# Kernel optimization log

Measured on AMD Instinct MI355X. Metric: run time of the kernel, lower is better.

The kernel has to match this reference:

```python
import jax, jax.numpy as jnp
import numpy as np

N_NODES = 4096
N_EDGES = 524288
IN_DIM = 6
EMB_N = 4
EMB_D = 8
EDGE_D = 1
HID = 64
N_HEADS = 4
LN_EPS = 1e-5


def _layernorm(h, g, b):
    m = jnp.mean(h, axis=-1, keepdims=True)
    v = jnp.mean(jnp.square(h - m), axis=-1, keepdims=True)
    return (h - m) * jax.lax.rsqrt(v + LN_EPS) * g + b


def setup_inputs() -> dict:
    key = jax.random.key(0)
    ks = jax.random.split(key, 16)
    s = lambda fan_in: 1.0 / np.sqrt(fan_in)
    inp = {
        'x': jax.random.normal(ks[0], (N_NODES, IN_DIM), jnp.float32),
        'edge_attr': jax.random.uniform(ks[1], (N_EDGES, EDGE_D), jnp.float32),
        'entity_emb': jax.random.normal(ks[2], (EMB_N, EMB_D), jnp.float32),
        'lin1_w': jax.random.uniform(ks[3], (HID, IN_DIM + EMB_D + EDGE_D), jnp.float32, -s(15), s(15)),
        'lin1_b': jnp.zeros((HID,), jnp.float32),
        'lay_w': jax.random.uniform(ks[4], (HID, HID), jnp.float32, -s(HID), s(HID)),
        'lay_b': jnp.zeros((HID,), jnp.float32),
        'ln_g': jnp.ones((HID,), jnp.float32),
        'ln_b': jnp.zeros((HID,), jnp.float32),
        'in_proj_w': jax.random.uniform(ks[5], (3 * HID, HID), jnp.float32, -s(HID), s(HID)),
        'in_proj_b': jnp.zeros((3 * HID,), jnp.float32),
        'out_proj_w': jax.random.uniform(ks[6], (HID, HID), jnp.float32, -s(HID), s(HID)),
        'out_proj_b': jnp.zeros((HID,), jnp.float32),
        'an_g': jnp.ones((HID,), jnp.float32),
        'an_b': jnp.zeros((HID,), jnp.float32),
        'out_w': jax.random.uniform(ks[7], (HID, HID), jnp.float32, -s(HID), s(HID)),
        'out_b': jnp.zeros((HID,), jnp.float32),
        'edge_index': jax.random.randint(ks[8], (2, N_EDGES), 0, N_NODES, jnp.int64),
        'entity_type': jax.random.randint(ks[9], (N_NODES,), 0, EMB_N, jnp.int64),
    }
    return inp


def reference(x, edge_attr, entity_emb, lin1_w, lin1_b, lay_w, lay_b, ln_g, ln_b,
              in_proj_w, in_proj_b, out_proj_w, out_proj_b, an_g, an_b, out_w, out_b,
              edge_index, entity_type):
    # --- EmbedConv ---
    # concat node features with entity embedding: [N, 6+8]
    xe = jnp.concatenate([x, entity_emb[entity_type]], axis=-1)
    src, dst = edge_index[0], edge_index[1]
    # gather source nodes + edge attr: [E, 15]
    msg = jnp.concatenate([xe[src], edge_attr], axis=-1)
    msg = _layernorm(jax.nn.relu(msg @ lin1_w.T + lin1_b), ln_g, ln_b)
    # layer_N = 1 extra layer, shared LayerNorm
    msg = _layernorm(jax.nn.relu(msg @ lay_w.T + lay_b), ln_g, ln_b)
    # scatter-add aggregate into destination nodes: [N, 64]
    h = jax.ops.segment_sum(msg, dst, num_segments=N_NODES)
    # --- MultiheadAttention over all nodes as one sequence (eval: no dropout) ---
    qkv = h @ in_proj_w.T + in_proj_b  # [N, 3H]
    q, k, v = jnp.split(qkv, 3, axis=-1)
    hd = HID // N_HEADS
    q = q.reshape(N_NODES, N_HEADS, hd).transpose(1, 0, 2)  # [h, n, d]
    k = k.reshape(N_NODES, N_HEADS, hd).transpose(1, 0, 2)
    v = v.reshape(N_NODES, N_HEADS, hd).transpose(1, 0, 2)
    scores = jnp.einsum('hnd,hmd->hnm', q, k) / np.sqrt(hd)
    attn = jax.nn.softmax(scores, axis=-1)
    o = jnp.einsum('hnm,hmd->hnd', attn, v).transpose(1, 0, 2).reshape(N_NODES, HID)
    o = o @ out_proj_w.T + out_proj_b
    h = _layernorm(h + o, an_g, an_b)
    # --- output layer ---
    return h @ out_w.T + out_b
```

## Files before the change

kernel.cpp:

```cpp
#include <hip/hip_runtime.h>

#define N_NODES 4096
#define N_EDGES 524288
#define HID 64

typedef short short8 __attribute__((ext_vector_type(8)));
typedef float f32x4 __attribute__((ext_vector_type(4)));
typedef float f32x16 __attribute__((ext_vector_type(16)));

__device__ __forceinline__ float bcastf(float v, int l) {
    return __int_as_float(__builtin_amdgcn_readlane(__float_as_int(v), l));
}

__device__ __forceinline__ void wave_sum2(float& a, float& b) {
    #pragma unroll
    for (int off = 32; off > 0; off >>= 1) {
        a += __shfl_xor(a, off, 64);
        b += __shfl_xor(b, off, 64);
    }
}

__device__ __forceinline__ short f2bf(float f) {
    unsigned u = __float_as_uint(f);
    u = u + 0x7FFFu + ((u >> 16) & 1u);
    return (short)(u >> 16);
}
__device__ __forceinline__ float bf2f(short s) {
    return __uint_as_float(((unsigned)(unsigned short)s) << 16);
}
__device__ __forceinline__ void split_cheap(float f, short& hi, short& lo) {
    unsigned u = __float_as_uint(f);
    unsigned hb = u & 0xffff0000u;
    float lof = f - __uint_as_float(hb);
    hi = (short)(u >> 16);
    lo = (short)(__float_as_uint(lof) >> 16);
}

__global__ void hist_prep(const float* __restrict__ x, const float* __restrict__ emb,
                          const int* __restrict__ etype, const int* __restrict__ ei,
                          const float* __restrict__ w1, const float* __restrict__ b1,
                          const float* __restrict__ w2, const float* __restrict__ lng,
                          const float* __restrict__ lnb, const float* __restrict__ b2,
                          const float* __restrict__ ipw,
                          float* __restrict__ A1, int* __restrict__ cnt, int* __restrict__ rank,
                          unsigned short* __restrict__ w2fh, unsigned short* __restrict__ w2fl,
                          unsigned short* __restrict__ ipfh, unsigned short* __restrict__ ipfl,
                          float* __restrict__ b2p, float* __restrict__ w14p) {
    int tid = blockIdx.x * 256 + threadIdx.x;
    int d = ei[N_EDGES + tid];
    rank[tid] = atomicAdd(&cnt[d], 1);
    if (tid < N_NODES * 64) {
        int n = tid >> 6, f = tid & 63;
        const float* wr = w1 + f * 15;
        float acc = b1[f];
        #pragma unroll
        for (int k = 0; k < 6; k++) acc = fmaf(x[n * 6 + k], wr[k], acc);
        int e = etype[n];
        #pragma unroll
        for (int k = 0; k < 8; k++) acc = fmaf(emb[e * 8 + k], wr[6 + k], acc);
        A1[tid] = acc;
    }
    if (tid < 4096) {
        int idx = tid >> 9, ln = (tid >> 3) & 63, j = tid & 7;
        int mm = ln & 15, qq = ln >> 4;
        int g = idx >> 1, tt = idx & 1;
        int col = tt * 32 + qq * 8 + j;
        float w = w2[(g * 16 + mm) * 64 + col] * lng[col];
        short hi = f2bf(w);
        w2fh[tid] = (unsigned short)hi;
        w2fl[tid] = (unsigned short)f2bf(w - bf2f(hi));
    }
    if (tid < 12288) {
        int idx = tid >> 9, ln = (tid >> 3) & 63, j = tid & 7;
        int mm = ln & 15, qq = ln >> 4;
        int og = idx >> 1, tt = idx & 1;
        float w = ipw[(og * 16 + mm) * 64 + tt * 32 + qq * 8 + j];
        short hi = f2bf(w);
        ipfh[tid] = (unsigned short)hi;
        ipfl[tid] = (unsigned short)f2bf(w - bf2f(hi));
    }
    if (tid < 64) {
        float acc = b2[tid];
        for (int c = 0; c < 64; c++) acc = fmaf(w2[tid * 64 + c], lnb[c], acc);
        b2p[tid] = acc;
        w14p[tid] = w1[tid * 15 + 14];
    }
}

__global__ void __launch_bounds__(256) scatter_scan(
        const int* __restrict__ cnt, const int* __restrict__ ei,
        const float* __restrict__ edge_attr, const int* __restrict__ rank,
        int* __restrict__ bnd,
        int* __restrict__ ssrc, float* __restrict__ sea) {
    __shared__ int lbnd[4096];
    __shared__ int wsum[4];
    int t = threadIdx.x;
    int base = t * 16;
    int v16[16];
    int T = 0;
    #pragma unroll
    for (int j = 0; j < 16; j++) { v16[j] = cnt[base + j]; T += v16[j]; }
    int inc = T;
    int l = t & 63;
    #pragma unroll
    for (int off = 1; off < 64; off <<= 1) {
        int v = __shfl_up(inc, off, 64);
        if (l >= off) inc += v;
    }
    if (l == 63) wsum[t >> 6] = inc;
    __syncthreads();
    int wo = 0;
    for (int w = 0; w < (t >> 6); w++) wo += wsum[w];
    int run = wo + inc - T;
    #pragma unroll
    for (int j = 0; j < 16; j++) {
        lbnd[base + j] = run;
        run += v16[j];
    }
    if (blockIdx.x == 0) {
        #pragma unroll
        for (int j = 0; j < 16; j++) bnd[base + j] = lbnd[base + j];
        if (t == 255) bnd[4096] = run;
    }
    __syncthreads();
    int e = blockIdx.x * 256 + t;
    int d = ei[N_EDGES + e];
    int pos = lbnd[d] + rank[e];
    ssrc[pos] = ei[e];
    sea[pos] = edge_attr[e];
}

__global__ void __launch_bounds__(256, 4) edge_gather_mfma(
        const float* __restrict__ A1,
        const int* __restrict__ ssrc, const float* __restrict__ sea,
        const int* __restrict__ bnd,
        const unsigned short* __restrict__ w2fh, const unsigned short* __restrict__ w2fl,
        const float* __restrict__ w14p, const float* __restrict__ b2p,
        const float* __restrict__ lg, const float* __restrict__ lb,
        float* __restrict__ h) {
    __shared__ uint4 lw2h4[512];
    __shared__ uint4 lw2l4[512];
    int tid = threadIdx.x;
    {
        const uint4* gh = (const uint4*)w2fh;
        const uint4* gl = (const uint4*)w2fl;
        lw2h4[tid] = gh[tid];
        lw2h4[tid + 256] = gh[tid + 256];
        lw2l4[tid] = gl[tid];
        lw2l4[tid + 256] = gl[tid + 256];
    }
    const unsigned short* lw2h = (const unsigned short*)lw2h4;
    const unsigned short* lw2l = (const unsigned short*)lw2l4;

    int lane = tid & 63;
    int wv = tid >> 6;
    int m = lane & 15;
    int q = lane >> 4;

    float w14f[16];
    {
        float4 wa = *(const float4*)(w14p + q * 8);
        float4 wb = *(const float4*)(w14p + q * 8 + 4);
        float4 wc = *(const float4*)(w14p + 32 + q * 8);
        float4 wd = *(const float4*)(w14p + 32 + q * 8 + 4);
        w14f[0] = wa.x; w14f[1] = wa.y; w14f[2] = wa.z; w14f[3] = wa.w;
        w14f[4] = wb.x; w14f[5] = wb.y; w14f[6] = wb.z; w14f[7] = wb.w;
        w14f[8] = wc.x; w14f[9] = wc.y; w14f[10] = wc.z; w14f[11] = wc.w;
        w14f[12] = wd.x; w14f[13] = wd.y; w14f[14] = wd.z; w14f[15] = wd.w;
    }
    float b2v[4];
    #pragma unroll
    for (int g = 0; g < 4; g++) b2v[g] = b2p[g * 16 + m];
    float lgv = lg[lane], lbv = lb[lane];

    int node = blockIdx.x * 4 + wv;
    int start = bnd[node], end = bnd[node + 1];
    int ntiles = (end - start + 15) >> 4;
    float acc[4] = {0.f, 0.f, 0.f, 0.f};
    __syncthreads();

    int srcn = 0; float eav = 0.f;
    if (ntiles > 0) {
        int ec = start + m; if (ec >= end) ec = end - 1;
        srcn = ssrc[ec]; eav = sea[ec];
    }
    for (int t = 0; t < ntiles; t++) {
        int base = start + t * 16;
        const float* ar = A1 + srcn * 64 + q * 8;
        float4 va = *(const float4*)(ar);
        float4 vb = *(const float4*)(ar + 4);
        float4 vc = *(const float4*)(ar + 32);
        float4 vd = *(const float4*)(ar + 36);
        int srcn_n = srcn; float eav_n = eav;
        if (t + 1 < ntiles) {
            int e2 = base + 16 + m; if (e2 >= end) e2 = end - 1;
            srcn_n = ssrc[e2]; eav_n = sea[e2];
        }
        float v[16] = {va.x, va.y, va.z, va.w, vb.x, vb.y, vb.z, vb.w,
                       vc.x, vc.y, vc.z, vc.w, vd.x, vd.y, vd.z, vd.w};
        float s = 0.f, s2 = 0.f;
        #pragma unroll
        for (int j = 0; j < 16; j++) {
            float u = fmaxf(fmaf(w14f[j], eav, v[j]), 0.f);
            v[j] = u;
            s += u;
            s2 = fmaf(u, u, s2);
        }
        s += __shfl_xor(s, 16, 64);  s2 += __shfl_xor(s2, 16, 64);
        s += __shfl_xor(s, 32, 64);  s2 += __shfl_xor(s2, 32, 64);
        float mean = s * (1.f / 64.f);
        float var = s2 * (1.f / 64.f) - mean * mean;
        float rs = rsqrtf(var + 1e-5f);
        float a0 = -mean * rs;
        short8 a2h[2], a2l[2];
        #pragma unroll
        for (int t2 = 0; t2 < 2; t2++)
            #pragma unroll
            for (int j = 0; j < 8; j++) {
                short hi, lo;
                split_cheap(fmaf(v[t2 * 8 + j], rs, a0), hi, lo);
                a2h[t2][j] = hi;
                a2l[t2][j] = lo;
            }
        int ob = (t >> 20);
        float s_[4] = {0, 0, 0, 0}, s2_[4] = {0, 0, 0, 0};
        float t2v[4][4];
        #pragma unroll
        for (int g = 0; g < 4; g++) {
            f32x4 c = {0.f, 0.f, 0.f, 0.f};
            #pragma unroll
            for (int t2 = 0; t2 < 2; t2++) {
                short8 bh = *(const short8*)(lw2h + ((g * 2 + t2) * 64 + lane + ob) * 8);
                short8 bl = *(const short8*)(lw2l + ((g * 2 + t2) * 64 + lane + ob) * 8);
                c = __builtin_amdgcn_mfma_f32_16x16x32_bf16(a2l[t2], bh, c, 0, 0, 0);
                c = __builtin_amdgcn_mfma_f32_16x16x32_bf16(a2h[t2], bl, c, 0, 0, 0);
                c = __builtin_amdgcn_mfma_f32_16x16x32_bf16(a2h[t2], bh, c, 0, 0, 0);
            }
            #pragma unroll
            for (int i = 0; i < 4; i++) {
                float vv = fmaxf(c[i] + b2v[g], 0.f);
                t2v[g][i] = vv;
                s_[i] += vv;
                s2_[i] = fmaf(vv, vv, s2_[i]);
            }
        }
        #pragma unroll
        for (int off = 1; off < 16; off <<= 1)
            #pragma unroll
            for (int i = 0; i < 4; i++) {
                s_[i] += __shfl_xor(s_[i], off, 64);
                s2_[i] += __shfl_xor(s2_[i], off, 64);
            }
        #pragma unroll
        for (int i = 0; i < 4; i++) {
            float mean2 = s_[i] * (1.f / 64.f);
            float var2 = s2_[i] * (1.f / 64.f) - mean2 * mean2;
            float rs2 = rsqrtf(var2 + 1e-5f);
            bool valid = (base + q * 4 + i) < end;
            #pragma unroll
            for (int g = 0; g < 4; g++) {
                float z = (t2v[g][i] - mean2) * rs2;
                if (valid) acc[g] += z;
            }
        }
        srcn = srcn_n; eav = eav_n;
    }
    #pragma unroll
    for (int g = 0; g < 4; g++) {
        acc[g] += __shfl_xor(acc[g], 16, 64);
        acc[g] += __shfl_xor(acc[g], 32, 64);
    }
    float a01 = (q & 1) ? acc[1] : acc[0];
    float a23 = (q & 1) ? acc[3] : acc[2];
    float av = (q & 2) ? a23 : a01;
    h[node * 64 + lane] = lgv * av + (float)(end - start) * lbv;
}

__global__ void __launch_bounds__(256) qkv_mfma(
        const float* __restrict__ h, const float* __restrict__ b,
        const unsigned short* __restrict__ ipfh, const unsigned short* __restrict__ ipfl,
        unsigned short* __restrict__ qhp, unsigned short* __restrict__ qlp,
        unsigned short* __restrict__ khp, unsigned short* __restrict__ klp,
        unsigned short* __restrict__ vT) {
    int lane = threadIdx.x & 63;
    int wv = threadIdx.x >> 6;
    int m = lane & 15;
    int q = lane >> 4;
    int wid = blockIdx.x * 4 + wv;
    int tile = wid / 12;
    int og = wid - tile * 12;
    short8 bh[2], bl[2];
    #pragma unroll
    for (int t = 0; t < 2; t++) {
        bh[t] = *(const short8*)(ipfh + ((og * 2 + t) * 64 + lane) * 8);
        bl[t] = *(const short8*)(ipfl + ((og * 2 + t) * 64 + lane) * 8);
    }
    f32x4 c = {0.f, 0.f, 0.f, 0.f};
    #pragma unroll
    for (int t = 0; t < 2; t++) {
        const float* hr = h + (tile * 16 + m) * 64 + t * 32 + q * 8;
        float4 f0 = *(const float4*)hr;
        float4 f1 = *(const float4*)(hr + 4);
        float av8[8] = {f0.x, f0.y, f0.z, f0.w, f1.x, f1.y, f1.z, f1.w};
        short8 ah, al;
        #pragma unroll
        for (int j = 0; j < 8; j++) {
            short hi, lo;
            split_cheap(av8[j], hi, lo);
            ah[j] = hi;
            al[j] = lo;
        }
        c = __builtin_amdgcn_mfma_f32_16x16x32_bf16(al, bh[t], c, 0, 0, 0);
        c = __builtin_amdgcn_mfma_f32_16x16x32_bf16(ah, bl[t], c, 0, 0, 0);
        c = __builtin_amdgcn_mfma_f32_16x16x32_bf16(ah, bh[t], c, 0, 0, 0);
    }
    int o = og * 16 + m;
    float bias = b[o];
    #pragma unroll
    for (int r = 0; r < 4; r++) {
        int node = tile * 16 + q * 4 + r;
        float val = c[r] + bias;
        if (og < 4) {
            float aq = val * (0.25f * 1.44269504f);
            size_t idx = ((size_t)(og * N_NODES + node)) * 16 + m;
            short hi = f2bf(aq);
            qhp[idx] = (unsigned short)hi;
            qlp[idx] = (unsigned short)f2bf(aq - bf2f(hi));
        } else if (og < 8) {
            size_t idx = ((size_t)((og - 4) * N_NODES + node)) * 16 + m;
            short hi = f2bf(val);
            khp[idx] = (unsigned short)hi;
            klp[idx] = (unsigned short)f2bf(val - bf2f(hi));
        } else {
            int feat = (og - 8) * 16 + m;
            vT[(size_t)feat * N_NODES + node] = (unsigned short)f2bf(val);
        }
    }
}

__global__ void __launch_bounds__(256) attn_mfma(
        const unsigned short* __restrict__ qhp, const unsigned short* __restrict__ qlp,
        const unsigned short* __restrict__ khp, const unsigned short* __restrict__ klp,
        const unsigned short* __restrict__ vT,
        float* __restrict__ part_o, float* __restrict__ part_ml) {
    int lane = threadIdx.x & 63;
    int wv = threadIdx.x >> 6;
    int l31 = lane & 31;
    int hi = lane >> 5;
    const short8 vones = {0x3F80, 0x3F80, 0x3F80, 0x3F80, 0x3F80, 0x3F80, 0x3F80, 0x3F80};

    int wid = blockIdx.x * 4 + wv;
    int kc = wid & 7;
    int wqt = (wid >> 3) & 127;
    int head = wid >> 10;

    int qrow = wqt * 32 + l31;
    short8 aqh = *(const short8*)(qhp + ((size_t)(head * N_NODES + qrow)) * 16 + hi * 8);
    short8 aql = *(const short8*)(qlp + ((size_t)(head * N_NODES + qrow)) * 16 + hi * 8);

    const unsigned short* khb = khp + (size_t)head * N_NODES * 16;
    const unsigned short* klb = klp + (size_t)head * N_NODES * 16;
    const unsigned short* vtb = vT + (size_t)(head * 16 + (l31 & 15)) * N_NODES;

    float mS = -3e38f;
    f32x16 Ot = {0.f, 0.f, 0.f, 0.f, 0.f, 0.f, 0.f, 0.f,
                 0.f, 0.f, 0.f, 0.f, 0.f, 0.f, 0.f, 0.f};

    size_t koff = ((size_t)(kc * 512 + l31)) * 16 + hi * 8;
    short8 bkh = *(const short8*)(khb + koff);
    short8 bkl = *(const short8*)(klb + koff);

    for (int bb = 0; bb < 16; bb++) {
        int n0 = kc * 512 + bb * 32;
        int nbb = (bb + 1 < 16) ? (bb + 1) : 15;
        size_t koffn = ((size_t)(kc * 512 + nbb * 32 + l31)) * 16 + hi * 8;
        short8 nkh = *(const short8*)(khb + koffn);
        short8 nkl = *(const short8*)(klb + koffn);
        f32x16 S = {0.f, 0.f, 0.f, 0.f, 0.f, 0.f, 0.f, 0.f,
                    0.f, 0.f, 0.f, 0.f, 0.f, 0.f, 0.f, 0.f};
        S = __builtin_amdgcn_mfma_f32_32x32x16_bf16(bkh, aql, S, 0, 0, 0);
        S = __builtin_amdgcn_mfma_f32_32x32x16_bf16(bkl, aqh, S, 0, 0, 0);
        S = __builtin_amdgcn_mfma_f32_32x32x16_bf16(bkh, aqh, S, 0, 0, 0);
        float mr = S[0];
        #pragma unroll
        for (int r = 1; r < 16; r++) mr = fmaxf(mr, S[r]);
        mr = fmaxf(mr, __shfl_xor(mr, 32, 64));
        if (!__all(mr <= mS)) {
            float mn = fmaxf(mS, mr);
            float alpha = exp2f(mS - mn);
            mS = mn;
            #pragma unroll
            for (int r = 0; r < 9; r++) Ot[r] *= alpha;
        }
        float p[16];
        #pragma unroll
        for (int r = 0; r < 16; r++) p[r] = exp2f(S[r] - mS);
        unsigned w0, w1, w2, w3, u0, u1, u2, u3;
        asm("v_cvt_pk_bf16_f32 %0, %1, %2" : "=v"(w0) : "v"(p[0]), "v"(p[1]));
        asm("v_cvt_pk_bf16_f32 %0, %1, %2" : "=v"(w1) : "v"(p[2]), "v"(p[3]));
        asm("v_cvt_pk_bf16_f32 %0, %1, %2" : "=v"(w2) : "v"(p[4]), "v"(p[5]));
        asm("v_cvt_pk_bf16_f32 %0, %1, %2" : "=v"(w3) : "v"(p[6]), "v"(p[7]));
        asm("v_cvt_pk_bf16_f32 %0, %1, %2" : "=v"(u0) : "v"(p[8]), "v"(p[9]));
        asm("v_cvt_pk_bf16_f32 %0, %1, %2" : "=v"(u1) : "v"(p[10]), "v"(p[11]));
        asm("v_cvt_pk_bf16_f32 %0, %1, %2" : "=v"(u2) : "v"(p[12]), "v"(p[13]));
        asm("v_cvt_pk_bf16_f32 %0, %1, %2" : "=v"(u3) : "v"(p[14]), "v"(p[15]));
        asm("v_permlane32_swap_b32 %0, %1" : "+v"(w0), "+v"(w2));
        asm("v_permlane32_swap_b32 %0, %1" : "+v"(w1), "+v"(w3));
        asm("v_permlane32_swap_b32 %0, %1" : "+v"(u0), "+v"(u2));
        asm("v_permlane32_swap_b32 %0, %1" : "+v"(u1), "+v"(u3));
        union { unsigned u[4]; short8 s; } pf0, pf1;
        pf0.u[0] = w0; pf0.u[1] = w1; pf0.u[2] = w2; pf0.u[3] = w3;
        pf1.u[0] = u0; pf1.u[1] = u1; pf1.u[2] = u2; pf1.u[3] = u3;
        short8 v0, v1;
        if (l31 < 16) {
            v0 = *(const short8*)(vtb + n0 + hi * 8);
            v1 = *(const short8*)(vtb + n0 + 16 + hi * 8);
        } else if (l31 == 16) {
            v0 = vones; v1 = vones;
        } else {
            v0 = (short8)0; v1 = (short8)0;
        }
        Ot = __builtin_amdgcn_mfma_f32_32x32x16_bf16(v0, pf0.s, Ot, 0, 0, 0);
        Ot = __builtin_amdgcn_mfma_f32_32x32x16_bf16(v1, pf1.s, Ot, 0, 0, 0);
        bkh = nkh; bkl = nkl;
    }
    int qt16 = wqt * 2 + (l31 >> 4);
    int qi = l31 & 15;
    size_t pb = ((size_t)(head * 8 + kc) * 256 + qt16) * 256;
    f32x4 o0 = {Ot[0], Ot[1], Ot[2], Ot[3]};
    f32x4 o1 = {Ot[4], Ot[5], Ot[6], Ot[7]};
    *(f32x4*)(part_o + pb + qi * 16 + hi * 4) = o0;
    *(f32x4*)(part_o + pb + qi * 16 + 8 + hi * 4) = o1;
    if (lane < 32) {
        size_t mb = ((size_t)(head * 8 + kc) * 256 + qt16) * 32;
        part_ml[mb + qi] = mS;
        part_ml[mb + 16 + qi] = Ot[8];
    }
}

__global__ void post_kernel(const float* __restrict__ h,
                            const float* __restrict__ part_o, const float* __restrict__ part_ml,
                            const float* __restrict__ opw, const float* __restrict__ opb,
                            const float* __restrict__ ag, const float* __restrict__ ab,
                            const float* __restrict__ ow, const float* __restrict__ ob,
                            float* __restrict__ out) {
    __shared__ float wl1[64 * 65];
    __shared__ float wl2[64 * 65];
    for (int i = threadIdx.x; i < 4096; i += blockDim.x) {
        int r = i >> 6, c = i & 63;
        wl1[r * 65 + c] = opw[i];
        wl2[r * 65 + c] = ow[i];
    }
    __syncthreads();
    int lane = threadIdx.x & 63;
    int n = blockIdx.x * 4 + (threadIdx.x >> 6);
    int j = lane;
    int head = j >> 4, d = j & 15;
    int qt = n >> 4, qi = n & 15;
    float M = -3e38f, L = 0.f, Ov = 0.f;
    #pragma unroll
    for (int c = 0; c < 8; c++) {
        size_t base = ((size_t)(head * 8 + c) * 256 + qt);
        float mc = part_ml[base * 32 + qi];
        float lc = part_ml[base * 32 + 16 + qi];
        float ov = part_o[base * 256 + qi * 16 + d];
        if (mc > M) {
            float sc = exp2f(M - mc);
            M = mc;
            L = L * sc + lc;
            Ov = Ov * sc + ov;
        } else {
            float sc = exp2f(mc - M);
            L = fmaf(lc, sc, L);
            Ov = fmaf(ov, sc, Ov);
        }
    }
    float oj = Ov / L;
    float acc = opb[j];
    #pragma unroll
    for (int k = 0; k < 64; k++) acc = fmaf(wl1[j * 65 + k], bcastf(oj, k), acc);
    float r = h[n * 64 + j] + acc;
    float s = r, s2 = r * r;
    wave_sum2(s, s2);
    float mean = s * (1.f / 64.f);
    float var = s2 * (1.f / 64.f) - mean * mean;
    float hn = (r - mean) * rsqrtf(var + 1e-5f) * ag[j] + ab[j];
    float acc2 = ob[j];
    #pragma unroll
    for (int k = 0; k < 64; k++) acc2 = fmaf(wl2[j * 65 + k], bcastf(hn, k), acc2);
    out[n * 64 + j] = acc2;
}

extern "C" void kernel_launch(void* const* d_in, const int* in_sizes, int n_in,
                              void* d_out, int out_size, void* d_ws, size_t ws_size,
                              hipStream_t stream) {
    const float* x        = (const float*)d_in[0];
    const float* edge_attr= (const float*)d_in[1];
    const float* emb      = (const float*)d_in[2];
    const float* lin1_w   = (const float*)d_in[3];
    const float* lin1_b   = (const float*)d_in[4];
    const float* lay_w    = (const float*)d_in[5];
    const float* lay_b    = (const float*)d_in[6];
    const float* ln_g     = (const float*)d_in[7];
    const float* ln_b     = (const float*)d_in[8];
    const float* ipw      = (const float*)d_in[9];
    const float* ipb      = (const float*)d_in[10];
    const float* opw      = (const float*)d_in[11];
    const float* opb      = (const float*)d_in[12];
    const float* ang      = (const float*)d_in[13];
    const float* anb      = (const float*)d_in[14];
    const float* ow       = (const float*)d_in[15];
    const float* ob       = (const float*)d_in[16];
    const int*   ei       = (const int*)d_in[17];
    const int*   et       = (const int*)d_in[18];

    char* wsb = (char*)d_ws;
    size_t off = 0;
    float* A1             = (float*)(wsb + off);          off += 1048576;
    float* h              = (float*)(wsb + off);          off += 1048576;
    unsigned short* qhp   = (unsigned short*)(wsb + off); off += 524288;
    unsigned short* qlp   = (unsigned short*)(wsb + off); off += 524288;
    unsigned short* khp   = (unsigned short*)(wsb + off); off += 524288;
    unsigned short* klp   = (unsigned short*)(wsb + off); off += 524288;
    unsigned short* vT    = (unsigned short*)(wsb + off); off += 524288;
    float* part_o         = (float*)(wsb + off);          off += 8388608;
    float* part_ml        = (float*)(wsb + off);          off += 1048576;
    int*   cnt            = (int*)(wsb + off);            off += 16384;
    int*   bnd            = (int*)(wsb + off);            off += 16388;
    off = (off + 255) & ~(size_t)255;
    int*   rank           = (int*)(wsb + off);            off += 2097152;
    int*   ssrc           = (int*)(wsb + off);            off += 2097152;
    float* sea            = (float*)(wsb + off);          off += 2097152;
    unsigned short* w2fh  = (unsigned short*)(wsb + off); off += 8192;
    unsigned short* w2fl  = (unsigned short*)(wsb + off); off += 8192;
    unsigned short* ipfh  = (unsigned short*)(wsb + off); off += 24576;
    unsigned short* ipfl  = (unsigned short*)(wsb + off); off += 24576;
    float* b2p            = (float*)(wsb + off);          off += 256;
    float* w14p           = (float*)(wsb + off);          off += 256;

    (void)hipMemsetAsync(cnt, 0, 4096 * sizeof(int), stream);
    hist_prep<<<2048, 256, 0, stream>>>(x, emb, et, ei, lin1_w, lin1_b, lay_w, ln_g, ln_b,
                                        lay_b, ipw, A1, cnt, rank, w2fh, w2fl, ipfh, ipfl,
                                        b2p, w14p);
    scatter_scan<<<2048, 256, 0, stream>>>(cnt, ei, edge_attr, rank, bnd, ssrc, sea);
    edge_gather_mfma<<<1024, 256, 0, stream>>>(A1, ssrc, sea, bnd, w2fh, w2fl,
                                               w14p, b2p, ln_g, ln_b, h);
    qkv_mfma<<<768, 256, 0, stream>>>(h, ipb, ipfh, ipfl, qhp, qlp, khp, klp, vT);
    attn_mfma<<<1024, 256, 0, stream>>>(qhp, qlp, khp, klp, vT, part_o, part_ml);
    post_kernel<<<1024, 256, 0, stream>>>(h, part_o, part_ml, opw, opb, ang, anb, ow, ob,
                                          (float*)d_out);
}
```

Baseline: 224.7 us.

## Restructure edge gather MFMA to transposed layout with persistent node loop

The edge kernel now swaps the MFMA operand order so each output column holds one edge, which lets the second LayerNorm reduce across lanes once per tile instead of four times, and accumulates 16 features per lane. The A1 row gather for the next tile is prefetched one iteration ahead. bf16 hi/lo splitting uses packed v_cvt_pk_bf16_f32, and the scan reads counts with int4 loads. The grid shrinks to 768 blocks looping over nodes, with launch bounds lowered to 3 blocks per SM. The larger accumulator arrays and the prefetch raise register pressure, and writing h only from m==0 lanes produces narrow scalar stores.

```diff
diff --git a/kernel.cpp b/kernel.cpp
--- a/kernel.cpp
+++ b/kernel.cpp
@@ -34,6 +34,23 @@
     float lof = f - __uint_as_float(hb);
     hi = (short)(u >> 16);
     lo = (short)(__float_as_uint(lof) >> 16);
+}
+
+__device__ __forceinline__ void pack_plane8(const float* vv, short8& ah, short8& al) {
+    union { unsigned u[4]; short8 s; } Uh, Ul;
+    #pragma unroll
+    for (int i = 0; i < 4; i++) {
+        unsigned hw;
+        asm("v_cvt_pk_bf16_f32 %0, %1, %2" : "=v"(hw) : "v"(vv[2 * i]), "v"(vv[2 * i + 1]));
+        float he = __uint_as_float(hw << 16);
+        float ho = __uint_as_float(hw & 0xffff0000u);
+        float le = vv[2 * i] - he;
+        float lo_ = vv[2 * i + 1] - ho;
+        unsigned lw;
+        asm("v_cvt_pk_bf16_f32 %0, %1, %2" : "=v"(lw) : "v"(le), "v"(lo_));
+        Uh.u[i] = hw; Ul.u[i] = lw;
+    }
+    ah = Uh.s; al = Ul.s;
 }
 
 __global__ void hist_prep(const float* __restrict__ x, const float* __restrict__ emb,
@@ -99,7 +116,12 @@
     int v16[16];
     int T = 0;
     #pragma unroll
-    for (int j = 0; j < 16; j++) { v16[j] = cnt[base + j]; T += v16[j]; }
+    for (int j4 = 0; j4 < 4; j4++) {
+        int4 c4 = ((const int4*)cnt)[t * 4 + j4];
+        v16[j4 * 4 + 0] = c4.x; v16[j4 * 4 + 1] = c4.y;
+        v16[j4 * 4 + 2] = c4.z; v16[j4 * 4 + 3] = c4.w;
+        T += c4.x + c4.y + c4.z + c4.w;
+    }
     int inc = T;
     int l = t & 63;
     #pragma unroll
@@ -130,7 +152,7 @@
     sea[pos] = edge_attr[e];
 }
 
-__global__ void __launch_bounds__(256, 4) edge_gather_mfma(
+__global__ void __launch_bounds__(256, 3) edge_gather_mfma(
         const float* __restrict__ A1,
         const int* __restrict__ ssrc, const float* __restrict__ sea,
         const int* __restrict__ bnd,
@@ -168,112 +190,117 @@
         w14f[8] = wc.x; w14f[9] = wc.y; w14f[10] = wc.z; w14f[11] = wc.w;
         w14f[12] = wd.x; w14f[13] = wd.y; w14f[14] = wd.z; w14f[15] = wd.w;
     }
-    float b2v[4];
-    #pragma unroll
-    for (int g = 0; g < 4; g++) b2v[g] = b2p[g * 16 + m];
-    float lgv = lg[lane], lbv = lb[lane];
-
-    int node = blockIdx.x * 4 + wv;
-    int start = bnd[node], end = bnd[node + 1];
-    int ntiles = (end - start + 15) >> 4;
-    float acc[4] = {0.f, 0.f, 0.f, 0.f};
+    float b2v[16];
+    #pragma unroll
+    for (int g = 0; g < 4; g++) {
+        float4 bb = *(const float4*)(b2p + g * 16 + q * 4);
+        b2v[g * 4 + 0] = bb.x; b2v[g * 4 + 1] = bb.y;
+        b2v[g * 4 + 2] = bb.z; b2v[g * 4 + 3] = bb.w;
+    }
     __syncthreads();
 
-    int srcn = 0; float eav = 0.f;
-    if (ntiles > 0) {
-        int ec = start + m; if (ec >= end) ec = end - 1;
-        srcn = ssrc[ec]; eav = sea[ec];
-    }
-    for (int t = 0; t < ntiles; t++) {
-        int base = start + t * 16;
-        const float* ar = A1 + srcn * 64 + q * 8;
-        float4 va = *(const float4*)(ar);
-        float4 vb = *(const float4*)(ar + 4);
-        float4 vc = *(const float4*)(ar + 32);
-        float4 vd = *(const float4*)(ar + 36);
-        int srcn_n = srcn; float eav_n = eav;
-        if (t + 1 < ntiles) {
-            int e2 = base + 16 + m; if (e2 >= end) e2 = end - 1;
-            srcn_n = ssrc[e2]; eav_n = sea[e2];
-        }
-        float v[16] = {va.x, va.y, va.z, va.w, vb.x, vb.y, vb.z, vb.w,
-                       vc.x, vc.y, vc.z, vc.w, vd.x, vd.y, vd.z, vd.w};
-        float s = 0.f, s2 = 0.f;
-        #pragma unroll
-        for (int j = 0; j < 16; j++) {
-            float u = fmaxf(fmaf(w14f[j], eav, v[j]), 0.f);
-            v[j] = u;
-            s += u;
-            s2 = fmaf(u, u, s2);
-        }
-        s += __shfl_xor(s, 16, 64);  s2 += __shfl_xor(s2, 16, 64);
-        s += __shfl_xor(s, 32, 64);  s2 += __shfl_xor(s2, 32, 64);
-        float mean = s * (1.f / 64.f);
-        float var = s2 * (1.f / 64.f) - mean * mean;
-        float rs = rsqrtf(var + 1e-5f);
-        float a0 = -mean * rs;
-        short8 a2h[2], a2l[2];
-        #pragma unroll
-        for (int t2 = 0; t2 < 2; t2++)
+    for (int node = blockIdx.x * 4 + wv; node < N_NODES; node += 3072) {
+        int start = bnd[node], end = bnd[node + 1];
+        int ntiles = (end - start + 15) >> 4;
+        float acc[16];
+        #pragma unroll
+        for (int i = 0; i < 16; i++) acc[i] = 0.f;
+
+        int srcn = 0; float eav = 0.f;
+        float4 va = {0,0,0,0}, vb = {0,0,0,0}, vc = {0,0,0,0}, vd = {0,0,0,0};
+        if (ntiles > 0) {
+            int ec = start + m; if (ec >= end) ec = end - 1;
+            srcn = ssrc[ec]; eav = sea[ec];
+            const float* ar = A1 + srcn * 64 + q * 8;
+            va = *(const float4*)(ar);
+            vb = *(const float4*)(ar + 4);
+            vc = *(const float4*)(ar + 32);
+            vd = *(const float4*)(ar + 36);
+        }
+        for (int t = 0; t < ntiles; t++) {
+            int base = start + t * 16;
+            float v[16] = {va.x, va.y, va.z, va.w, vb.x, vb.y, vb.z, vb.w,
+                           vc.x, vc.y, vc.z, vc.w, vd.x, vd.y, vd.z, vd.w};
+            float eavc = eav;
+            if (t + 1 < ntiles) {
+                int e2 = base + 16 + m; if (e2 >= end) e2 = end - 1;
+                int srcn2 = ssrc[e2]; eav = sea[e2];
+                const float* ar2 = A1 + srcn2 * 64 + q * 8;
+                va = *(const float4*)(ar2);
+                vb = *(const float4*)(ar2 + 4);
+                vc = *(const float4*)(ar2 + 32);
+                vd = *(const float4*)(ar2 + 36);
+            }
+            float s = 0.f, s2 = 0.f;
             #pragma unroll
-            for (int j = 0; j < 8; j++) {
-                short hi, lo;
-                split_cheap(fmaf(v[t2 * 8 + j], rs, a0), hi, lo);
-                a2h[t2][j] = hi;
-                a2l[t2][j] = lo;
+            for (int j = 0; j < 16; j++) {
+                float u = fmaxf(fmaf(w14f[j], eavc, v[j]), 0.f);
+                v[j] = u;
+                s += u;
+                s2 = fmaf(u, u, s2);
             }
-        int ob = (t >> 20);
-        float s_[4] = {0, 0, 0, 0}, s2_[4] = {0, 0, 0, 0};
-        float t2v[4][4];
-        #pragma unroll
-        for (int g = 0; g < 4; g++) {
-            f32x4 c = {0.f, 0.f, 0.f, 0.f};
+            s += __shfl_xor(s, 16, 64);  s2 += __shfl_xor(s2, 16, 64);
+            s += __shfl_xor(s, 32, 64);  s2 += __shfl_xor(s2, 32, 64);
+            float mean = s * (1.f / 64.f);
+            float var = s2 * (1.f / 64.f) - mean * mean;
+            float rs = rsqrtf(var + 1e-5f);
+            float a0 = -mean * rs;
             #pragma unroll
-            for (int t2 = 0; t2 < 2; t2++) {
-                short8 bh = *(const short8*)(lw2h + ((g * 2 + t2) * 64 + lane + ob) * 8);
-                short8 bl = *(const short8*)(lw2l + ((g * 2 + t2) * 64 + lane + ob) * 8);
-                c = __builtin_amdgcn_mfma_f32_16x16x32_bf16(a2l[t2], bh, c, 0, 0, 0);
-                c = __builtin_amdgcn_mfma_f32_16x16x32_bf16(a2h[t2], bl, c, 0, 0, 0);
-                c = __builtin_amdgcn_mfma_f32_16x16x32_bf16(a2h[t2], bh, c, 0, 0, 0);
+            for (int j = 0; j < 16; j++) v[j] = fmaf(v[j], rs, a0);
+            short8 a2h[2], a2l[2];
+            pack_plane8(v, a2h[0], a2l[0]);
+            pack_plane8(v + 8, a2h[1], a2l[1]);
+            int ob = (t >> 20);
+            float s_ = 0.f, s2_ = 0.f;
+            float t2v[16];
+            #pragma unroll
+            for (int g = 0; g < 4; g++) {
+                f32x4 c = {0.f, 0.f, 0.f, 0.f};
+                #pragma unroll
+                for (int t2 = 0; t2 < 2; t2++) {
+                    short8 bh = *(const short8*)(lw2h + ((g * 2 + t2) * 64 + lane + ob) * 8);
+                    short8 bl = *(const short8*)(lw2l + ((g * 2 + t2) * 64 + lane + ob) * 8);
+                    c = __builtin_amdgcn_mfma_f32_16x16x32_bf16(bh, a2l[t2], c, 0, 0, 0);
+                    c = __builtin_amdgcn_mfma_f32_16x16x32_bf16(bl, a2h[t2], c, 0, 0, 0);
+                    c = __builtin_amdgcn_mfma_f32_16x16x32_bf16(bh, a2h[t2], c, 0, 0, 0);
+                }
+                #pragma unroll
+                for (int r = 0; r < 4; r++) {
+                    float vv = fmaxf(c[r] + b2v[g * 4 + r], 0.f);
+                    t2v[g * 4 + r] = vv;
+                    s_ += vv;
+                    s2_ = fmaf(vv, vv, s2_);
+                }
             }
-            #pragma unroll
-            for (int i = 0; i < 4; i++) {
-                float vv = fmaxf(c[i] + b2v[g], 0.f);
-                t2v[g][i] = vv;
-                s_[i] += vv;
-                s2_[i] = fmaf(vv, vv, s2_[i]);
+            s_ += __shfl_xor(s_, 16, 64);  s2_ += __shfl_xor(s2_, 16, 64);
+            s_ += __shfl_xor(s_, 32, 64);  s2_ += __shfl_xor(s2_, 32, 64);
+            float mean2 = s_ * (1.f / 64.f);
+            float var2 = s2_ * (1.f / 64.f) - mean2 * mean2;
+            float rs2 = rsqrtf(var2 + 1e-5f);
+            float a02 = -mean2 * rs2;
+            if (base + m < end) {
+                #pragma unroll
+                for (int i = 0; i < 16; i++) acc[i] += fmaf(t2v[i], rs2, a02);
             }
         }
         #pragma unroll
         for (int off = 1; off < 16; off <<= 1)
             #pragma unroll
-            for (int i = 0; i < 4; i++) {
-                s_[i] += __shfl_xor(s_[i], off, 64);
-                s2_[i] += __shfl_xor(s2_[i], off, 64);
-            }
-        #pragma unroll
-        for (int i = 0; i < 4; i++) {
-            float mean2 = s_[i] * (1.f / 64.f);
-            float var2 = s2_[i] * (1.f / 64.f) - mean2 * mean2;
-            float rs2 = rsqrtf(var2 + 1e-5f);
-            bool valid = (base + q * 4 + i) < end;
+            for (int i = 0; i < 16; i++) acc[i] += __shfl_xor(acc[i], off, 64);
+        if (m == 0) {
+            float deg = (float)(end - start);
             #pragma unroll
             for (int g = 0; g < 4; g++) {
-                float z = (t2v[g][i] - mean2) * rs2;
-                if (valid) acc[g] += z;
+                float4 lgv = *(const float4*)(lg + g * 16 + q * 4);
+                float4 lbv = *(const float4*)(lb + g * 16 + q * 4);
+                float* hp = h + node * 64 + g * 16 + q * 4;
+                hp[0] = lgv.x * acc[g * 4 + 0] + deg * lbv.x;
+                hp[1] = lgv.y * acc[g * 4 + 1] + deg * lbv.y;
+                hp[2] = lgv.z * acc[g * 4 + 2] + deg * lbv.z;
+                hp[3] = lgv.w * acc[g * 4 + 3] + deg * lbv.w;
             }
         }
-        srcn = srcn_n; eav = eav_n;
-    }
-    #pragma unroll
-    for (int g = 0; g < 4; g++) {
-        acc[g] += __shfl_xor(acc[g], 16, 64);
-        acc[g] += __shfl_xor(acc[g], 32, 64);
-    }
-    float a01 = (q & 1) ? acc[1] : acc[0];
-    float a23 = (q & 1) ? acc[3] : acc[2];
-    float av = (q & 2) ? a23 : a01;
-    h[node * 64 + lane] = lgv * av + (float)(end - start) * lbv;
+    }
 }
 
 __global__ void __launch_bounds__(256) qkv_mfma(
@@ -543,8 +570,8 @@
                                         lay_b, ipw, A1, cnt, rank, w2fh, w2fl, ipfh, ipfl,
                                         b2p, w14p);
     scatter_scan<<<2048, 256, 0, stream>>>(cnt, ei, edge_attr, rank, bnd, ssrc, sea);
-    edge_gather_mfma<<<1024, 256, 0, stream>>>(A1, ssrc, sea, bnd, w2fh, w2fl,
-                                               w14p, b2p, ln_g, ln_b, h);
+    edge_gather_mfma<<<768, 256, 0, stream>>>(A1, ssrc, sea, bnd, w2fh, w2fl,
+                                              w14p, b2p, ln_g, ln_b, h);
     qkv_mfma<<<768, 256, 0, stream>>>(h, ipb, ipfh, ipfl, qhp, qlp, khp, klp, vT);
     attn_mfma<<<1024, 256, 0, stream>>>(qhp, qlp, khp, klp, vT, part_o, part_ml);
     post_kernel<<<1024, 256, 0, stream>>>(h, part_o, part_ml, opw, opb, ang, anb, ow, ob,
```

New measurement: 221.7 us. Within noise of the previous version (-1.3%).
